# Optimization experiments

Hardware: AMD Instinct MI355X
Metric: run time of the kernel (lower is better)

## Reference

```python
import jax, jax.numpy as jnp
import numpy as np

B, S, E, H = 8, 1024, 1024, 16
D = E // H  # head_dim = 64


def setup_inputs() -> dict:
    key = jax.random.key(0)
    ks = jax.random.split(key, 8)
    scale = 1.0 / np.sqrt(E)
    return {
        "query": jax.random.normal(ks[0], (B, S, E), jnp.float32),
        "key": jax.random.normal(ks[1], (B, S, E), jnp.float32),
        "value": jax.random.normal(ks[2], (B, S, E), jnp.float32),
        "q_w": jax.random.normal(ks[3], (E, E), jnp.float32) * scale,
        "q_b": jnp.zeros((E,), jnp.float32),
        "k_w": jax.random.normal(ks[4], (E, E), jnp.float32) * scale,
        "k_b": jnp.zeros((E,), jnp.float32),
        "v_w": jax.random.normal(ks[5], (E, E), jnp.float32) * scale,
        "v_b": jnp.zeros((E,), jnp.float32),
        "out_w": jax.random.normal(ks[6], (E, E), jnp.float32) * scale,
        "out_b": jnp.zeros((E,), jnp.float32),
    }


def reference(query, key, value, q_w, q_b, k_w, k_b, v_w, v_b, out_w, out_b):
    b = query.shape[0]
    scaling = 1.0 / jnp.sqrt(jnp.asarray(D, query.dtype))
    # torch Linear: x @ W.T + b; split heads -> (b, H, S, D)
    def proj(x, w, bias):
        y = jnp.einsum('bse,fe->bsf', x, w) + bias
        return y.reshape(b, -1, H, D).transpose(0, 2, 1, 3)
    q = proj(query, q_w, q_b)
    k = proj(key, k_w, k_b)
    v = proj(value, v_w, v_b)
    scores = jnp.einsum('bhqd,bhkd->bhqk', q, k) * scaling
    attn_weights = jax.nn.softmax(scores, axis=-1)
    # dropout is identity in eval mode (deterministic reference)
    context = jnp.einsum('bhqk,bhkd->bhqd', attn_weights, v)
    context = context.transpose(0, 2, 1, 3).reshape(b, -1, E)
    output = jnp.einsum('bse,fe->bsf', context, out_w) + out_b
    return (attn_weights, output)
```

## Files before the change

kernel.cpp:

```cpp
#include <hip/hip_runtime.h>

typedef __attribute__((ext_vector_type(8))) short short8;
typedef __attribute__((ext_vector_type(4))) float f32x4;
typedef unsigned short u16;

#define DEVI __device__ __forceinline__

DEVI u16 f2bf(float f) {
  unsigned u = __float_as_uint(f);
  unsigned r = (u + 0x7fffu + ((u >> 16) & 1u)) >> 16;
  return (u16)r;
}

DEVI void gl2lds16(const void* g, void* l) {
  __builtin_amdgcn_global_load_lds((const __attribute__((address_space(1))) void*)g,
                                   (__attribute__((address_space(3))) void*)l, 16, 0, 0);
}

template<int ROWS, int BKE>
DEVI void stage_bf16(const u16* __restrict__ g, int ld, u16* lds, int tid) {
  constexpr int CPR = BKE / 8;
  constexpr int CH  = ROWS * CPR;
  const int wave = tid >> 6, lane = tid & 63;
#pragma unroll
  for (int i = 0; i < CH / 256; i++) {
    int c = (i * 4 + wave) * 64 + lane;
    int row = c / CPR;
    int colb = (c % CPR) * 16;
    gl2lds16((const char*)g + (long)row * ld * 2 + colb, (char*)lds + (long)c * 16);
  }
}

template<int FM, int FN, int BKE>
DEVI void kstep(const u16* Alds, const u16* Blds, int lane, int wr, int wc, int kk,
                f32x4 (*acc)[FN]) {
  const int ro = lane & 15, ko = kk + (lane >> 4) * 8;
  short8 a[FM], b[FN];
#pragma unroll
  for (int m = 0; m < FM; m++) a[m] = *(const short8*)(Alds + (wr + m * 16 + ro) * BKE + ko);
#pragma unroll
  for (int n = 0; n < FN; n++) b[n] = *(const short8*)(Blds + (wc + n * 16 + ro) * BKE + ko);
#pragma unroll
  for (int m = 0; m < FM; m++)
#pragma unroll
    for (int n = 0; n < FN; n++)
      acc[m][n] = __builtin_amdgcn_mfma_f32_16x16x32_bf16(a[m], b[n], acc[m][n], 0, 0, 0);
}

struct CvtArgs {
  const float* s[7];
  u16* d[7];
  int n8[7];
};

__global__ __launch_bounds__(256) void cvt_all(CvtArgs a) {
  const int t = blockIdx.y;
  const int n = a.n8[t];
  const float* __restrict__ s = a.s[t];
  u16* __restrict__ d = a.d[t];
  for (long i = blockIdx.x * 256 + threadIdx.x; i < n; i += (long)gridDim.x * 256) {
    float4 v0 = ((const float4*)s)[2 * i];
    float4 v1 = ((const float4*)s)[2 * i + 1];
    ushort4 h0, h1;
    h0.x = f2bf(v0.x); h0.y = f2bf(v0.y); h0.z = f2bf(v0.z); h0.w = f2bf(v0.w);
    h1.x = f2bf(v1.x); h1.y = f2bf(v1.y); h1.z = f2bf(v1.z); h1.w = f2bf(v1.w);
    ((ushort4*)d)[2 * i] = h0;
    ((ushort4*)d)[2 * i + 1] = h1;
  }
}

struct Biases { const float* p[3]; };

__global__ __launch_bounds__(256) void proj3_kernel(const u16* __restrict__ Xb,
                                                    const u16* __restrict__ Wb,
                                                    Biases bs,
                                                    u16* __restrict__ Outb) {
  __shared__ u16 Alds[128 * 64];
  __shared__ u16 Blds[128 * 64];
  const int tid = threadIdx.x, lane = tid & 63, w = tid >> 6;
  const int wr = (w >> 1) * 64, wc = (w & 1) * 64;
  const int z = blockIdx.z;
  const u16* X = Xb + (long)z * 8388608;
  const u16* W = Wb + (long)z * 1048576;
  const float* bias = bs.p[z];
  u16* Out = Outb + (long)z * 8388608;
  const long rowB = (long)blockIdx.x * 128;
  const int colB = blockIdx.y * 128;
  f32x4 acc[4][4] = {};
  for (int k0 = 0; k0 < 1024; k0 += 64) {
    stage_bf16<128, 64>(X + rowB * 1024 + k0, 1024, Alds, tid);
    stage_bf16<128, 64>(W + (long)colB * 1024 + k0, 1024, Blds, tid);
    __syncthreads();
    kstep<4, 4, 64>(Alds, Blds, lane, wr, wc, 0, acc);
    kstep<4, 4, 64>(Alds, Blds, lane, wr, wc, 32, acc);
    __syncthreads();
  }
  const int ro = (lane >> 4) * 4, co = lane & 15;
  const float sc = (z == 0) ? 0.125f : 1.0f;
  if (z < 2) {
#pragma unroll
    for (int n = 0; n < 4; n++) {
      const int col = colB + wc + n * 16 + co;
      const float bv = bias[col];
      const int h = col >> 6, d = col & 63;
#pragma unroll
      for (int m = 0; m < 4; m++)
#pragma unroll
        for (int j = 0; j < 4; j++) {
          long r = rowB + wr + m * 16 + ro + j;
          long bq = r >> 10, s = r & 1023;
          Out[(((bq * 16 + h) * 1024 + s) << 6) + d] = f2bf((acc[m][n][j] + bv) * sc);
        }
    }
  } else {
#pragma unroll
    for (int n = 0; n < 4; n++) {
      const int col = colB + wc + n * 16 + co;
      const float bv = bias[col];
      const long h = col >> 6, d = col & 63;
#pragma unroll
      for (int m = 0; m < 4; m++) {
        long r0 = rowB + wr + m * 16 + ro;
        long bq = r0 >> 10, s = r0 & 1023;
        ushort4 pk;
        pk.x = f2bf(acc[m][n][0] + bv);
        pk.y = f2bf(acc[m][n][1] + bv);
        pk.z = f2bf(acc[m][n][2] + bv);
        pk.w = f2bf(acc[m][n][3] + bv);
        *(ushort4*)(Out + (((bq * 16 + h) << 16) | (d << 10) | s)) = pk;
      }
    }
  }
}

__global__ __launch_bounds__(256) void flash_kernel(const u16* __restrict__ Q,
                                                    const u16* __restrict__ K,
                                                    const u16* __restrict__ Vt,
                                                    float* __restrict__ attn,
                                                    u16* __restrict__ Ctx) {
  __shared__ u16 Klds[2 * 64 * 64];
  __shared__ u16 Vlds[2 * 64 * 64];
  __shared__ u16 Plds[128 * 64];
  const int tid = threadIdx.x, lane = tid & 63, w = tid >> 6;
  const int z = blockIdx.x;
  const int rowB = blockIdx.y * 128;
  const int b = z >> 4, h = z & 15;
  const u16* Qb  = Q  + (long)z * 65536 + (long)rowB * 64;
  const u16* Kb  = K  + (long)z * 65536;
  const u16* Vtb = Vt + (long)z * 65536;
  const int ro = lane & 15, ko8 = (lane >> 4) * 8;
  const int qw = w * 32;

  short8 aq[2][2];
#pragma unroll
  for (int m = 0; m < 2; m++)
#pragma unroll
    for (int kt = 0; kt < 2; kt++)
      aq[m][kt] = *(const short8*)(Qb + (qw + m * 16 + ro) * 64 + kt * 32 + ko8);

  float lsum[8];
#pragma unroll
  for (int i = 0; i < 8; i++) lsum[i] = 0.0f;

  stage_bf16<64, 64>(Kb, 64, Klds, tid);
  __syncthreads();
  for (int kb = 0; kb < 16; kb++) {
    const int cur = kb & 1, nxt = cur ^ 1;
    if (kb < 15) stage_bf16<64, 64>(Kb + (kb + 1) * 4096, 64, Klds + nxt * 4096, tid);
    const u16* Kc = Klds + cur * 4096;
    f32x4 acc[2][4] = {};
#pragma unroll
    for (int kt = 0; kt < 2; kt++) {
      short8 bfr[4];
#pragma unroll
      for (int n = 0; n < 4; n++)
        bfr[n] = *(const short8*)(Kc + (n * 16 + ro) * 64 + kt * 32 + ko8);
#pragma unroll
      for (int m = 0; m < 2; m++)
#pragma unroll
        for (int n = 0; n < 4; n++)
          acc[m][n] = __builtin_amdgcn_mfma_f32_16x16x32_bf16(aq[m][kt], bfr[n], acc[m][n], 0, 0, 0);
    }
#pragma unroll
    for (int m = 0; m < 2; m++)
#pragma unroll
      for (int j = 0; j < 4; j++) {
        const int i = m * 4 + j;
        lsum[i] += __expf(acc[m][0][j]) + __expf(acc[m][1][j]) +
                   __expf(acc[m][2][j]) + __expf(acc[m][3][j]);
      }
    __syncthreads();
  }
  float linv[8];
#pragma unroll
  for (int i = 0; i < 8; i++) {
    float s = lsum[i];
#pragma unroll
    for (int o = 8; o > 0; o >>= 1) s += __shfl_xor(s, o, 64);
    linv[i] = 1.0f / s;
  }

  f32x4 acc_o[2][4] = {};
  float* ab = attn + ((long)z << 20) + (long)rowB * 1024;
  stage_bf16<64, 64>(Kb, 64, Klds, tid);
  stage_bf16<64, 64>(Vtb, 1024, Vlds, tid);
  __syncthreads();
  for (int kb = 0; kb < 16; kb++) {
    const int cur = kb & 1, nxt = cur ^ 1;
    if (kb < 15) {
      stage_bf16<64, 64>(Kb + (kb + 1) * 4096, 64, Klds + nxt * 4096, tid);
      stage_bf16<64, 64>(Vtb + (kb + 1) * 64, 1024, Vlds + nxt * 4096, tid);
    }
    const u16* Kc = Klds + cur * 4096;
    const u16* Vc = Vlds + cur * 4096;
    f32x4 acc[2][4] = {};
#pragma unroll
    for (int kt = 0; kt < 2; kt++) {
      short8 bfr[4];
#pragma unroll
      for (int n = 0; n < 4; n++)
        bfr[n] = *(const short8*)(Kc + (n * 16 + ro) * 64 + kt * 32 + ko8);
#pragma unroll
      for (int m = 0; m < 2; m++)
#pragma unroll
        for (int n = 0; n < 4; n++)
          acc[m][n] = __builtin_amdgcn_mfma_f32_16x16x32_bf16(aq[m][kt], bfr[n], acc[m][n], 0, 0, 0);
    }
#pragma unroll
    for (int m = 0; m < 2; m++)
#pragma unroll
      for (int j = 0; j < 4; j++) {
        const int i = m * 4 + j;
        const int ql = qw + m * 16 + (lane >> 4) * 4 + j;
        float* rowp = ab + (long)ql * 1024 + kb * 64;
        u16* prow = Plds + ql * 64;
        const int sw = ((ql & 7) << 3);
#pragma unroll
        for (int n = 0; n < 4; n++) {
          const int col = n * 16 + (lane & 15);
          float p = __expf(acc[m][n][j]) * linv[i];
          __builtin_nontemporal_store(p, rowp + col);
          prow[col ^ sw] = f2bf(p);
        }
      }
    asm volatile("s_waitcnt lgkmcnt(0)" ::: "memory");
    __builtin_amdgcn_sched_barrier(0);
#pragma unroll
    for (int kt = 0; kt < 2; kt++) {
      short8 pa[2], bv[4];
#pragma unroll
      for (int m = 0; m < 2; m++) {
        const int row = qw + m * 16 + ro;
        pa[m] = *(const short8*)(Plds + row * 64 + ((kt * 32 + ko8) ^ ((row & 7) << 3)));
      }
#pragma unroll
      for (int n = 0; n < 4; n++)
        bv[n] = *(const short8*)(Vc + (n * 16 + ro) * 64 + kt * 32 + ko8);
#pragma unroll
      for (int m = 0; m < 2; m++)
#pragma unroll
        for (int n = 0; n < 4; n++)
          acc_o[m][n] = __builtin_amdgcn_mfma_f32_16x16x32_bf16(pa[m], bv[n], acc_o[m][n], 0, 0, 0);
    }
    __syncthreads();
  }

  u16* cb = Ctx + ((long)b << 20) + (long)h * 64;
#pragma unroll
  for (int m = 0; m < 2; m++)
#pragma unroll
    for (int j = 0; j < 4; j++) {
      const long s = rowB + qw + m * 16 + (lane >> 4) * 4 + j;
#pragma unroll
      for (int n = 0; n < 4; n++)
        cb[s * 1024 + n * 16 + (lane & 15)] = f2bf(acc_o[m][n][j]);
    }
}

__global__ __launch_bounds__(256) void outb_kernel(const u16* __restrict__ Ctx,
                                                   const u16* __restrict__ W,
                                                   const float* __restrict__ bias,
                                                   float* __restrict__ Out) {
  __shared__ u16 Alds[128 * 64];
  __shared__ u16 Blds[128 * 64];
  const int tid = threadIdx.x, lane = tid & 63, w = tid >> 6;
  const int wr = (w >> 1) * 64, wc = (w & 1) * 64;
  const long rowB = (long)blockIdx.x * 128;
  const int colB = blockIdx.y * 128;
  f32x4 acc[4][4] = {};
  for (int k0 = 0; k0 < 1024; k0 += 64) {
    stage_bf16<128, 64>(Ctx + rowB * 1024 + k0, 1024, Alds, tid);
    stage_bf16<128, 64>(W + (long)colB * 1024 + k0, 1024, Blds, tid);
    __syncthreads();
    kstep<4, 4, 64>(Alds, Blds, lane, wr, wc, 0, acc);
    kstep<4, 4, 64>(Alds, Blds, lane, wr, wc, 32, acc);
    __syncthreads();
  }
  const int ro = (lane >> 4) * 4, co = lane & 15;
#pragma unroll
  for (int n = 0; n < 4; n++) {
    const int col = colB + wc + n * 16 + co;
    const float bv = bias[col];
#pragma unroll
    for (int m = 0; m < 4; m++)
#pragma unroll
      for (int j = 0; j < 4; j++) {
        long r = rowB + wr + m * 16 + ro + j;
        __builtin_nontemporal_store(acc[m][n][j] + bv, Out + r * 1024 + col);
      }
  }
}

extern "C" void kernel_launch(void* const* d_in, const int* in_sizes, int n_in,
                              void* d_out, int out_size, void* d_ws, size_t ws_size,
                              hipStream_t stream) {
  const float* query = (const float*)d_in[0];
  const float* key   = (const float*)d_in[1];
  const float* value = (const float*)d_in[2];
  const float* q_w   = (const float*)d_in[3];
  const float* q_b   = (const float*)d_in[4];
  const float* k_w   = (const float*)d_in[5];
  const float* k_b   = (const float*)d_in[6];
  const float* v_w   = (const float*)d_in[7];
  const float* v_b   = (const float*)d_in[8];
  const float* out_w = (const float*)d_in[9];
  const float* out_b = (const float*)d_in[10];

  const long MB = 1048576L;
  char* ws = (char*)d_ws;
  u16* Qp  = (u16*)(ws);
  u16* Kp  = (u16*)(ws + 16 * MB);
  u16* Vt  = (u16*)(ws + 32 * MB);
  u16* Qb  = (u16*)(ws + 48 * MB);
  u16* Kb  = (u16*)(ws + 64 * MB);
  u16* Vb  = (u16*)(ws + 80 * MB);
  u16* Ctx = (u16*)(ws + 64 * MB);
  u16* Wq  = (u16*)(ws + 96 * MB);
  u16* Wk  = (u16*)(ws + 98 * MB);
  u16* Wv  = (u16*)(ws + 100 * MB);
  u16* Wo  = (u16*)(ws + 102 * MB);

  float* attn = (float*)d_out;
  float* outp = (float*)d_out + 134217728L;

  CvtArgs ca;
  ca.s[0] = query; ca.d[0] = Qb; ca.n8[0] = 1048576;
  ca.s[1] = key;   ca.d[1] = Kb; ca.n8[1] = 1048576;
  ca.s[2] = value; ca.d[2] = Vb; ca.n8[2] = 1048576;
  ca.s[3] = q_w;   ca.d[3] = Wq; ca.n8[3] = 131072;
  ca.s[4] = k_w;   ca.d[4] = Wk; ca.n8[4] = 131072;
  ca.s[5] = v_w;   ca.d[5] = Wv; ca.n8[5] = 131072;
  ca.s[6] = out_w; ca.d[6] = Wo; ca.n8[6] = 131072;

  Biases bs;
  bs.p[0] = q_b; bs.p[1] = k_b; bs.p[2] = v_b;

  dim3 blk(256);
  cvt_all<<<dim3(2048, 7), blk, 0, stream>>>(ca);
  proj3_kernel<<<dim3(64, 8, 3), blk, 0, stream>>>(Qb, Wq, bs, Qp);
  flash_kernel<<<dim3(128, 8), blk, 0, stream>>>(Qp, Kp, Vt, attn, Ctx);
  outb_kernel<<<dim3(64, 8), blk, 0, stream>>>(Ctx, Wo, out_b, outp);
}
```

Baseline: 362.8 us.

## Deepen K prefetch, halve P scratch, and use vmcnt-gated barriers in flash kernel

Merges the K, V and P shared buffers into one 40KB LDS array. The first pass gets a 4-slot ring with a prefetch distance of two tiles, gated by vmcnt-based waits and raw s_barrier instead of __syncthreads. The second pass processes P in two 32-column halves so the P scratch shrinks to 128x32 with an XOR swizzle, and it adds a launch-bounds occupancy hint of 4 blocks. This is meant to hide global-load latency and raise occupancy, at the cost of fragile hand-counted vmcnt values that depend on how many loads stage_bf16 issues.

```diff
diff --git a/kernel.cpp b/kernel.cpp
--- a/kernel.cpp
+++ b/kernel.cpp
@@ -133,14 +133,13 @@
   }
 }
 
-__global__ __launch_bounds__(256) void flash_kernel(const u16* __restrict__ Q,
-                                                    const u16* __restrict__ K,
-                                                    const u16* __restrict__ Vt,
-                                                    float* __restrict__ attn,
-                                                    u16* __restrict__ Ctx) {
-  __shared__ u16 Klds[2 * 64 * 64];
-  __shared__ u16 Vlds[2 * 64 * 64];
-  __shared__ u16 Plds[128 * 64];
+__global__ __launch_bounds__(256, 4) void flash_kernel(const u16* __restrict__ Q,
+                                                       const u16* __restrict__ K,
+                                                       const u16* __restrict__ Vt,
+                                                       float* __restrict__ attn,
+                                                       u16* __restrict__ Ctx) {
+  __shared__ u16 lds[20480];
+  u16* const Pl = lds + 16384;
   const int tid = threadIdx.x, lane = tid & 63, w = tid >> 6;
   const int z = blockIdx.x;
   const int rowB = blockIdx.y * 128;
@@ -162,12 +161,8 @@
 #pragma unroll
   for (int i = 0; i < 8; i++) lsum[i] = 0.0f;
 
-  stage_bf16<64, 64>(Kb, 64, Klds, tid);
-  __syncthreads();
-  for (int kb = 0; kb < 16; kb++) {
-    const int cur = kb & 1, nxt = cur ^ 1;
-    if (kb < 15) stage_bf16<64, 64>(Kb + (kb + 1) * 4096, 64, Klds + nxt * 4096, tid);
-    const u16* Kc = Klds + cur * 4096;
+  auto p1_compute = [&](int kb) {
+    const u16* Kc = lds + (kb & 3) * 4096;
     f32x4 acc[2][4] = {};
 #pragma unroll
     for (int kt = 0; kt < 2; kt++) {
@@ -189,8 +184,28 @@
         lsum[i] += __expf(acc[m][0][j]) + __expf(acc[m][1][j]) +
                    __expf(acc[m][2][j]) + __expf(acc[m][3][j]);
       }
-    __syncthreads();
-  }
+    asm volatile("s_waitcnt lgkmcnt(0)" ::: "memory");
+    __builtin_amdgcn_sched_barrier(0);
+  };
+
+  stage_bf16<64, 64>(Kb, 64, lds, tid);
+  stage_bf16<64, 64>(Kb + 4096, 64, lds + 4096, tid);
+  for (int kb = 0; kb < 14; kb++) {
+    stage_bf16<64, 64>(Kb + (kb + 2) * 4096, 64, lds + ((kb + 2) & 3) * 4096, tid);
+    asm volatile("s_waitcnt vmcnt(4)" ::: "memory");
+    __builtin_amdgcn_s_barrier();
+    __builtin_amdgcn_sched_barrier(0);
+    p1_compute(kb);
+  }
+  asm volatile("s_waitcnt vmcnt(2)" ::: "memory");
+  __builtin_amdgcn_s_barrier();
+  __builtin_amdgcn_sched_barrier(0);
+  p1_compute(14);
+  asm volatile("s_waitcnt vmcnt(0)" ::: "memory");
+  __builtin_amdgcn_s_barrier();
+  __builtin_amdgcn_sched_barrier(0);
+  p1_compute(15);
+
   float linv[8];
 #pragma unroll
   for (int i = 0; i < 8; i++) {
@@ -202,17 +217,18 @@
 
   f32x4 acc_o[2][4] = {};
   float* ab = attn + ((long)z << 20) + (long)rowB * 1024;
-  stage_bf16<64, 64>(Kb, 64, Klds, tid);
-  stage_bf16<64, 64>(Vtb, 1024, Vlds, tid);
-  __syncthreads();
+  stage_bf16<64, 64>(Kb, 64, lds, tid);
+  stage_bf16<64, 64>(Vtb, 1024, lds + 8192, tid);
+  asm volatile("s_waitcnt vmcnt(0)" ::: "memory");
+  __builtin_amdgcn_s_barrier();
+  __builtin_amdgcn_sched_barrier(0);
   for (int kb = 0; kb < 16; kb++) {
-    const int cur = kb & 1, nxt = cur ^ 1;
     if (kb < 15) {
-      stage_bf16<64, 64>(Kb + (kb + 1) * 4096, 64, Klds + nxt * 4096, tid);
-      stage_bf16<64, 64>(Vtb + (kb + 1) * 64, 1024, Vlds + nxt * 4096, tid);
-    }
-    const u16* Kc = Klds + cur * 4096;
-    const u16* Vc = Vlds + cur * 4096;
+      stage_bf16<64, 64>(Kb + (kb + 1) * 4096, 64, lds + ((kb + 1) & 1) * 4096, tid);
+      stage_bf16<64, 64>(Vtb + (kb + 1) * 64, 1024, lds + (2 + ((kb + 1) & 1)) * 4096, tid);
+    }
+    const u16* Kc = lds + (kb & 1) * 4096;
+    const u16* Vc = lds + (2 + (kb & 1)) * 4096;
     f32x4 acc[2][4] = {};
 #pragma unroll
     for (int kt = 0; kt < 2; kt++) {
@@ -227,42 +243,48 @@
           acc[m][n] = __builtin_amdgcn_mfma_f32_16x16x32_bf16(aq[m][kt], bfr[n], acc[m][n], 0, 0, 0);
     }
 #pragma unroll
-    for (int m = 0; m < 2; m++)
-#pragma unroll
-      for (int j = 0; j < 4; j++) {
-        const int i = m * 4 + j;
-        const int ql = qw + m * 16 + (lane >> 4) * 4 + j;
-        float* rowp = ab + (long)ql * 1024 + kb * 64;
-        u16* prow = Plds + ql * 64;
-        const int sw = ((ql & 7) << 3);
-#pragma unroll
-        for (int n = 0; n < 4; n++) {
-          const int col = n * 16 + (lane & 15);
-          float p = __expf(acc[m][n][j]) * linv[i];
-          __builtin_nontemporal_store(p, rowp + col);
-          prow[col ^ sw] = f2bf(p);
+    for (int hh = 0; hh < 2; hh++) {
+#pragma unroll
+      for (int m = 0; m < 2; m++)
+#pragma unroll
+        for (int j = 0; j < 4; j++) {
+          const int i = m * 4 + j;
+          const int ql = qw + m * 16 + (lane >> 4) * 4 + j;
+          float* rowp = ab + (long)ql * 1024 + kb * 64 + hh * 32;
+          u16* prow = Pl + ql * 32;
+#pragma unroll
+          for (int nn = 0; nn < 2; nn++) {
+            const int n = hh * 2 + nn;
+            const int co = lane & 15;
+            const int ch = nn * 16 + co;
+            float p = __expf(acc[m][n][j]) * linv[i];
+            __builtin_nontemporal_store(p, rowp + ch);
+            prow[(((ch >> 3) ^ (ql & 3)) << 3) | (ch & 7)] = f2bf(p);
+          }
         }
+      asm volatile("s_waitcnt lgkmcnt(0)" ::: "memory");
+      __builtin_amdgcn_sched_barrier(0);
+      short8 pa[2], bv[4];
+#pragma unroll
+      for (int m = 0; m < 2; m++) {
+        const int row = qw + m * 16 + ro;
+        const int slot = (lane >> 4) ^ (row & 3);
+        pa[m] = *(const short8*)(Pl + row * 32 + slot * 8);
       }
+#pragma unroll
+      for (int n = 0; n < 4; n++)
+        bv[n] = *(const short8*)(Vc + (n * 16 + ro) * 64 + hh * 32 + ko8);
+#pragma unroll
+      for (int m = 0; m < 2; m++)
+#pragma unroll
+        for (int n = 0; n < 4; n++)
+          acc_o[m][n] = __builtin_amdgcn_mfma_f32_16x16x32_bf16(pa[m], bv[n], acc_o[m][n], 0, 0, 0);
+    }
     asm volatile("s_waitcnt lgkmcnt(0)" ::: "memory");
     __builtin_amdgcn_sched_barrier(0);
-#pragma unroll
-    for (int kt = 0; kt < 2; kt++) {
-      short8 pa[2], bv[4];
-#pragma unroll
-      for (int m = 0; m < 2; m++) {
-        const int row = qw + m * 16 + ro;
-        pa[m] = *(const short8*)(Plds + row * 64 + ((kt * 32 + ko8) ^ ((row & 7) << 3)));
-      }
-#pragma unroll
-      for (int n = 0; n < 4; n++)
-        bv[n] = *(const short8*)(Vc + (n * 16 + ro) * 64 + kt * 32 + ko8);
-#pragma unroll
-      for (int m = 0; m < 2; m++)
-#pragma unroll
-        for (int n = 0; n < 4; n++)
-          acc_o[m][n] = __builtin_amdgcn_mfma_f32_16x16x32_bf16(pa[m], bv[n], acc_o[m][n], 0, 0, 0);
-    }
-    __syncthreads();
+    asm volatile("s_waitcnt vmcnt(32)" ::: "memory");
+    __builtin_amdgcn_s_barrier();
+    __builtin_amdgcn_sched_barrier(0);
   }
 
   u16* cb = Ctx + ((long)b << 20) + (long)h * 64;
```

Measured after the change: 397.6 us. 9.6% more time.
